# Kernel tuning notes

Hardware: AMD Instinct MI355X
Metric: run time of the kernel (lower is better)

Reference implementation:

```python
import jax, jax.numpy as jnp
import numpy as np

QBITS = 8  # fake-quant bit width from q_config
DT_RANK = 128
D_STATE = 16


def fake_quant_tensor(x, bits=QBITS):
    """Per-tensor symmetric fake quantization (quantize-dequantize) with STE."""
    qmax = 2.0 ** (bits - 1) - 1.0
    s = jnp.maximum(jnp.max(jnp.abs(x)) / qmax, 1e-8)
    q = jnp.clip(jnp.round(x / s), -qmax - 1.0, qmax) * s
    return x + jax.lax.stop_gradient(q - x)


def fake_quant_per_channel(w, bits=QBITS):
    """Per-output-channel symmetric fake quantization for weights [out, in]."""
    qmax = 2.0 ** (bits - 1) - 1.0
    s = jnp.maximum(jnp.max(jnp.abs(w), axis=-1, keepdims=True) / qmax, 1e-8)
    q = jnp.clip(jnp.round(w / s), -qmax - 1.0, qmax) * s
    return w + jax.lax.stop_gradient(q - w)


def setup_inputs() -> dict:
    key = jax.random.key(0)
    ks = jax.random.split(key, 8)
    B, L, D_MODEL = 2, 4096, 2048
    d_inner = D_MODEL  # expand = 1.0
    x = jax.random.normal(ks[0], (B, L, D_MODEL), jnp.float32)
    prompt = 0.1 * jax.random.normal(ks[1], (B, L, D_STATE), jnp.float32)
    # x_proj: Linear(d_inner -> dt_rank + 2*d_state), no bias
    Wx = jax.random.normal(ks[2], (DT_RANK + 2 * D_STATE, d_inner), jnp.float32) / np.sqrt(d_inner)
    # dt_proj: Linear(dt_rank -> d_inner), with bias
    Wdt = jax.random.normal(ks[3], (d_inner, DT_RANK), jnp.float32) / np.sqrt(DT_RANK)
    bdt = 0.1 * jax.random.normal(ks[4], (d_inner,), jnp.float32)
    # S4D-real init for A_log, D skip param (standard Mamba selective-scan params)
    A_log = jnp.log(jnp.tile(jnp.arange(1, D_STATE + 1, dtype=jnp.float32), (d_inner, 1)))
    Dskip = jax.random.normal(ks[5], (d_inner,), jnp.float32)
    return dict(x=x, prompt=prompt, Wx=Wx, Wdt=Wdt, bdt=bdt, A_log=A_log, Dskip=Dskip)


def reference(x, prompt, Wx, Wdt, bdt, A_log, Dskip):
    # x_proj with fake-quantized weight, then split into dt / B / C
    x_dbl = jnp.einsum('bld,od->blo', x, fake_quant_per_channel(Wx))
    dts = x_dbl[..., :DT_RANK]
    Bs = x_dbl[..., DT_RANK:DT_RANK + D_STATE]
    Cs = x_dbl[..., DT_RANK + D_STATE:]
    # dt_proj with fake-quantized weight
    dts = jnp.einsum('blr,or->blo', dts, fake_quant_per_channel(Wdt)) + bdt
    # activation fake-quant of scan inputs
    u_q = fake_quant_tensor(x)          # [B, L, d_inner]
    dt_q = fake_quant_tensor(dts)       # [B, L, d_inner]
    B_q = fake_quant_tensor(Bs)         # [B, L, d_state]
    C_q = fake_quant_tensor(Cs + prompt)  # [B, L, d_state]
    # selective scan (quantized SSM weights A, D)
    A = -jnp.exp(fake_quant_per_channel(A_log))  # [d_inner, d_state]
    D_q = fake_quant_tensor(Dskip)               # [d_inner]
    dt = jax.nn.softplus(dt_q)

    def step(h, inp):
        u_t, dt_t, B_t, C_t = inp  # [B,d], [B,d], [B,n], [B,n]
        dA = jnp.exp(dt_t[:, :, None] * A)             # [B, d, n]
        dBu = (dt_t * u_t)[:, :, None] * B_t[:, None, :]
        h = dA * h + dBu                               # [B, d, n]
        y = jnp.einsum('bdn,bn->bd', h, C_t)
        return h, y

    Bsz, L, d = x.shape
    h0 = jnp.zeros((Bsz, d, D_STATE), x.dtype)
    xs = (jnp.swapaxes(u_q, 0, 1), jnp.swapaxes(dt, 0, 1),
          jnp.swapaxes(B_q, 0, 1), jnp.swapaxes(C_q, 0, 1))
    _, ys = jax.lax.scan(step, h0, xs)  # ys: [L, B, d]
    return jnp.swapaxes(ys, 0, 1) + u_q * D_q
```

## Files before the change

kernel.cpp:

```cpp
#include <hip/hip_runtime.h>
#include <hip/hip_bf16.h>

#define BSZ    2
#define LSEQ   4096
#define DMODEL 2048
#define DTR    128
#define DST    16
#define ODIM   160
#define MROWS  (BSZ*LSEQ)
#define CH     64
#define TT     (LSEQ/CH)
#define LOG2E  1.44269504088896340736f
#define LN2    0.69314718055994530942f

typedef short  short8  __attribute__((ext_vector_type(8)));
typedef float  floatx4 __attribute__((ext_vector_type(4)));

__device__ __forceinline__ unsigned short f2bf(float f) {
    unsigned u = __float_as_uint(f);
    u += 0x7fffu + ((u >> 16) & 1u);
    return (unsigned short)(u >> 16);
}
__device__ __forceinline__ float quantv(float x, float s, float inv_s) {
    float q = rintf(x * inv_s);
    q = fminf(fmaxf(q, -128.0f), 127.0f);
    return q * s;
}
__device__ __forceinline__ float softplus_fast(float v) {
    float t = __builtin_amdgcn_exp2f(-fabsf(v) * LOG2E);
    return fmaxf(v, 0.0f) + LN2 * __log2f(1.0f + t);
}
__device__ __forceinline__ float scale_from_bits(unsigned bits) {
    return fmaxf(__uint_as_float(bits) * (1.0f/127.0f), 1e-8f);
}
__device__ __forceinline__ int pidx(int r, int k, int K) {
    return (r >> 4)*(16*K) + ((k >> 5) << 9) + (((r & 15) + (((k & 31) >> 3) << 4)) << 3) + (k & 7);
}

#define PB_WX  160
#define PB_WDT 128
#define PB_A   128
#define PB_D   1
#define PREP_BLOCKS (PB_WX + PB_WDT + PB_A + PB_D)

__global__ __launch_bounds__(256) void k_prep(
    const float* __restrict__ Wx, const float* __restrict__ Wdt,
    const float* __restrict__ A_log, const float* __restrict__ Dskip,
    unsigned short* __restrict__ Wxq, unsigned short* __restrict__ Wdtq,
    float* __restrict__ a2, float* __restrict__ Dq)
{
    int bid = blockIdx.x, tid = threadIdx.x;
    __shared__ float red[256];
    if (bid < PB_WX) {
        int o = bid, base = o * DMODEL;
        float m = 0.0f;
        for (int i = tid; i < DMODEL; i += 256) m = fmaxf(m, fabsf(Wx[base+i]));
        red[tid] = m; __syncthreads();
        for (int s2 = 128; s2 > 0; s2 >>= 1) { if (tid < s2) red[tid] = fmaxf(red[tid], red[tid+s2]); __syncthreads(); }
        float s = fmaxf(red[0]*(1.0f/127.0f), 1e-8f), inv = 1.0f/s;
        for (int i = tid; i < DMODEL; i += 256)
            Wxq[pidx(o, i, DMODEL)] = f2bf(quantv(Wx[base+i], s, inv));
    } else if (bid < PB_WX + PB_WDT) {
        int n = (bid - PB_WX)*16 + (tid >> 4);
        int k0 = (tid & 15)*8;
        const float* src = Wdt + (size_t)n*DTR + k0;
        float4 v0 = *reinterpret_cast<const float4*>(src);
        float4 v1 = *reinterpret_cast<const float4*>(src + 4);
        float m = fmaxf(fmaxf(fmaxf(fabsf(v0.x), fabsf(v0.y)), fmaxf(fabsf(v0.z), fabsf(v0.w))),
                        fmaxf(fmaxf(fabsf(v1.x), fabsf(v1.y)), fmaxf(fabsf(v1.z), fabsf(v1.w))));
        for (int off = 1; off < 16; off <<= 1) m = fmaxf(m, __shfl_xor(m, off, 16));
        float s = fmaxf(m*(1.0f/127.0f), 1e-8f), inv = 1.0f/s;
        short8 o8;
        o8[0]=(short)f2bf(quantv(v0.x,s,inv)); o8[1]=(short)f2bf(quantv(v0.y,s,inv));
        o8[2]=(short)f2bf(quantv(v0.z,s,inv)); o8[3]=(short)f2bf(quantv(v0.w,s,inv));
        o8[4]=(short)f2bf(quantv(v1.x,s,inv)); o8[5]=(short)f2bf(quantv(v1.y,s,inv));
        o8[6]=(short)f2bf(quantv(v1.z,s,inv)); o8[7]=(short)f2bf(quantv(v1.w,s,inv));
        *reinterpret_cast<short8*>(Wdtq + pidx(n, k0, DTR)) = o8;
    } else if (bid < PB_WX + PB_WDT + PB_A) {
        int d = (bid - PB_WX - PB_WDT)*16 + (tid >> 4);
        int n = tid & 15;
        float v = A_log[d*DST + n];
        float m = fabsf(v);
        for (int off = 1; off < 16; off <<= 1) m = fmaxf(m, __shfl_xor(m, off, 16));
        float s = fmaxf(m*(1.0f/127.0f), 1e-8f);
        float q = quantv(v, s, 1.0f/s);
        a2[d*DST + n] = -expf(q) * LOG2E;
    } else {
        float m = 0.0f;
        for (int i = tid; i < DMODEL; i += 256) m = fmaxf(m, fabsf(Dskip[i]));
        red[tid] = m; __syncthreads();
        for (int s2 = 128; s2 > 0; s2 >>= 1) { if (tid < s2) red[tid] = fmaxf(red[tid], red[tid+s2]); __syncthreads(); }
        float s = fmaxf(red[0]*(1.0f/127.0f), 1e-8f), inv = 1.0f/s;
        for (int i = tid; i < DMODEL; i += 256) Dq[i] = quantv(Dskip[i], s, inv);
    }
}

__global__ __launch_bounds__(256) void k_mm1(
    const float* __restrict__ x, const unsigned short* __restrict__ Wxq,
    const float* __restrict__ prompt,
    unsigned short* __restrict__ xdblbf, float* __restrict__ xbc,
    unsigned* __restrict__ scales)
{
    int tid = threadIdx.x, w = tid >> 6, lane = tid & 63;
    int mrow = lane & 15, quad = lane >> 4;
    int mt = blockIdx.x, m0 = mt*16, k0 = w*512;
    floatx4 acc[10] = {};
    float xmax = 0.0f;
    const float* arow = x + (size_t)(m0 + mrow)*DMODEL + k0 + quad*8;
    for (int kk = 0; kk < 512; kk += 32) {
        const float4* ap = reinterpret_cast<const float4*>(arow + kk);
        float4 a0 = ap[0], a1 = ap[1];
        xmax = fmaxf(xmax, fmaxf(fmaxf(fabsf(a0.x), fabsf(a0.y)), fmaxf(fabsf(a0.z), fabsf(a0.w))));
        xmax = fmaxf(xmax, fmaxf(fmaxf(fabsf(a1.x), fabsf(a1.y)), fmaxf(fabsf(a1.z), fabsf(a1.w))));
        short8 af;
        af[0]=(short)f2bf(a0.x); af[1]=(short)f2bf(a0.y); af[2]=(short)f2bf(a0.z); af[3]=(short)f2bf(a0.w);
        af[4]=(short)f2bf(a1.x); af[5]=(short)f2bf(a1.y); af[6]=(short)f2bf(a1.z); af[7]=(short)f2bf(a1.w);
        int kcidx = (k0 + kk) >> 5;
        #pragma unroll
        for (int j = 0; j < 10; ++j) {
            short8 bf = *reinterpret_cast<const short8*>(Wxq + j*16*DMODEL + kcidx*512 + lane*8);
            acc[j] = __builtin_amdgcn_mfma_f32_16x16x32_bf16(af, bf, acc[j], 0, 0, 0);
        }
    }
    for (int off = 32; off; off >>= 1) xmax = fmaxf(xmax, __shfl_xor(xmax, off, 64));
    __shared__ float red[4*2560];
    __shared__ float redB[256], redC[256];
    __shared__ float wred[4];
    if (lane == 0) wred[w] = xmax;
    #pragma unroll
    for (int j = 0; j < 10; ++j) {
        float4 v = make_float4(acc[j][0], acc[j][1], acc[j][2], acc[j][3]);
        *reinterpret_cast<float4*>(&red[w*2560 + (j*16 + mrow)*16 + quad*4]) = v;
    }
    __syncthreads();
    float bmax = 0.0f, cmax = 0.0f;
    #pragma unroll
    for (int j = 0; j < 10; ++j) {
        int e = j*256 + tid;
        float v = red[e] + red[2560+e] + red[5120+e] + red[7680+e];
        int col = e >> 4, rowin = e & 15, row = m0 + rowin;
        if (col < DTR) {
            xdblbf[mt*16*DTR + ((col>>5)<<9) + ((rowin + (((col&31)>>3)<<4))<<3) + (col&7)] = f2bf(v);
        } else if (col < DTR + DST) {
            bmax = fmaxf(bmax, fabsf(v));
            xbc[(size_t)row*32 + (col - DTR)] = v;
        } else {
            v += prompt[(size_t)row*DST + (col - DTR - DST)];
            cmax = fmaxf(cmax, fabsf(v));
            xbc[(size_t)row*32 + 16 + (col - DTR - DST)] = v;
        }
    }
    redB[tid] = bmax; redC[tid] = cmax; __syncthreads();
    for (int s2 = 128; s2 > 0; s2 >>= 1) {
        if (tid < s2) { redB[tid] = fmaxf(redB[tid], redB[tid+s2]); redC[tid] = fmaxf(redC[tid], redC[tid+s2]); }
        __syncthreads();
    }
    if (tid == 0) {
        atomicMax(&scales[0], __float_as_uint(fmaxf(fmaxf(wred[0], wred[1]), fmaxf(wred[2], wred[3]))));
        atomicMax(&scales[1], __float_as_uint(redB[0]));
        atomicMax(&scales[2], __float_as_uint(redC[0]));
    }
}

__global__ __launch_bounds__(256) void k_mm2(
    const unsigned short* __restrict__ Ap, const unsigned short* __restrict__ Bp,
    const float* __restrict__ bdt, float* __restrict__ dts, unsigned* __restrict__ scales)
{
    int tid = threadIdx.x, w = tid >> 6, lane = tid & 63;
    int mrow = lane & 15, quad = lane >> 4;
    int mt = blockIdx.x >> 4, nt = blockIdx.x & 15;
    int mtile = mt*4 + w, m0 = mtile*16, n0 = nt*128;
    short8 afr[4];
    const unsigned short* ab = Ap + (size_t)mtile*16*DTR + lane*8;
    #pragma unroll
    for (int kc = 0; kc < 4; ++kc) afr[kc] = *reinterpret_cast<const short8*>(ab + (kc<<9));
    floatx4 acc[8] = {};
    #pragma unroll
    for (int j = 0; j < 8; ++j) {
        const unsigned short* bb = Bp + (size_t)(n0/16 + j)*16*DTR + lane*8;
        #pragma unroll
        for (int kc = 0; kc < 4; ++kc) {
            short8 bf = *reinterpret_cast<const short8*>(bb + (kc<<9));
            acc[j] = __builtin_amdgcn_mfma_f32_16x16x32_bf16(afr[kc], bf, acc[j], 0, 0, 0);
        }
    }
    float dmax = 0.0f;
    #pragma unroll
    for (int j = 0; j < 8; ++j) {
        int col = n0 + j*16 + mrow;
        float bv = bdt[col];
        #pragma unroll
        for (int r = 0; r < 4; ++r) {
            int row = m0 + quad*4 + r;
            float v = acc[j][r] + bv;
            dmax = fmaxf(dmax, fabsf(v));
            dts[(size_t)row*DMODEL + col] = v;
        }
    }
    for (int off = 32; off; off >>= 1) dmax = fmaxf(dmax, __shfl_xor(dmax, off, 64));
    __shared__ float wd[4];
    if (lane == 0) wd[w] = dmax;
    __syncthreads();
    if (tid == 0)
        atomicMax(&scales[3], __float_as_uint(fmaxf(fmaxf(wd[0], wd[1]), fmaxf(wd[2], wd[3]))));
}

__global__ __launch_bounds__(256) void k_scan1(
    const float* __restrict__ dts, const float* __restrict__ x,
    const float* __restrict__ xbc, const float* __restrict__ a2,
    const unsigned* __restrict__ scales,
    float* __restrict__ Aprod, float* __restrict__ hfin)
{
    int bid = blockIdx.x, tid = threadIdx.x;
    int b = bid >> 9, rem = bid & 511, dblk = rem >> 6, ch = rem & 63;
    int d = dblk*256 + tid, t0 = ch*TT;
    float s_u  = scale_from_bits(scales[0]), inv_su  = 1.0f/s_u;
    float s_B  = scale_from_bits(scales[1]), inv_sB  = 1.0f/s_B;
    float s_dt = scale_from_bits(scales[3]), inv_sdt = 1.0f/s_dt;
    float a2r[16];
    {
        const float4* ap = reinterpret_cast<const float4*>(a2 + (size_t)d*DST);
        float4 v0 = ap[0], v1 = ap[1], v2 = ap[2], v3 = ap[3];
        a2r[0]=v0.x; a2r[1]=v0.y; a2r[2]=v0.z; a2r[3]=v0.w;
        a2r[4]=v1.x; a2r[5]=v1.y; a2r[6]=v1.z; a2r[7]=v1.w;
        a2r[8]=v2.x; a2r[9]=v2.y; a2r[10]=v2.z; a2r[11]=v2.w;
        a2r[12]=v3.x; a2r[13]=v3.y; a2r[14]=v3.z; a2r[15]=v3.w;
    }
    float h[16];
    #pragma unroll
    for (int n = 0; n < 16; ++n) h[n] = 0.0f;
    float sdt = 0.0f;
    __shared__ __align__(16) float Bq_p[8*16];
    for (int sub = 0; sub < TT/8; ++sub) {
        int tbase = t0 + sub*8;
        if (tid < 128) {
            int tb = tid >> 4, n = tid & 15;
            Bq_p[tid] = quantv(xbc[(size_t)(b*LSEQ + tbase + tb)*32 + n], s_B, inv_sB);
        }
        float dtr[8], ur[8];
        const float* pD = dts + (size_t)(b*LSEQ + tbase)*DMODEL + d;
        const float* pX = x   + (size_t)(b*LSEQ + tbase)*DMODEL + d;
        #pragma unroll
        for (int r = 0; r < 8; ++r) { dtr[r] = pD[(size_t)r*DMODEL]; ur[r] = pX[(size_t)r*DMODEL]; }
        __syncthreads();
        #pragma unroll
        for (int r = 0; r < 8; ++r) {
            float dtq = quantv(dtr[r], s_dt, inv_sdt);
            float dtv = softplus_fast(dtq);
            float uq  = quantv(ur[r], s_u, inv_su);
            float dtu = dtv * uq;
            sdt += dtv;
            const float4* bq4 = reinterpret_cast<const float4*>(&Bq_p[r*16]);
            float4 b0 = bq4[0], b1 = bq4[1], b2 = bq4[2], b3 = bq4[3];
            float bq[16] = { b0.x,b0.y,b0.z,b0.w, b1.x,b1.y,b1.z,b1.w,
                             b2.x,b2.y,b2.z,b2.w, b3.x,b3.y,b3.z,b3.w };
            #pragma unroll
            for (int n = 0; n < 16; ++n) {
                float dA = __builtin_amdgcn_exp2f(a2r[n]*dtv);
                h[n] = fmaf(dA, h[n], dtu*bq[n]);
            }
        }
        __syncthreads();
    }
    size_t ob = ((size_t)((b*CH + ch)*DMODEL + d))*DST;
    #pragma unroll
    for (int i = 0; i < 4; ++i) {
        float4 av = make_float4(__builtin_amdgcn_exp2f(a2r[4*i+0]*sdt),
                                __builtin_amdgcn_exp2f(a2r[4*i+1]*sdt),
                                __builtin_amdgcn_exp2f(a2r[4*i+2]*sdt),
                                __builtin_amdgcn_exp2f(a2r[4*i+3]*sdt));
        float4 hv = make_float4(h[4*i+0], h[4*i+1], h[4*i+2], h[4*i+3]);
        *reinterpret_cast<float4*>(Aprod + ob + 4*i) = av;
        *reinterpret_cast<float4*>(hfin  + ob + 4*i) = hv;
    }
}

__global__ __launch_bounds__(256) void k_mid(
    float* __restrict__ Aprod, const float* __restrict__ hfin)
{
    int f = blockIdx.x*256 + threadIdx.x;
    int b = f >> 15, dn = f & 32767;
    size_t base = (size_t)b*CH*32768 + dn;
    float h = 0.0f;
    #pragma unroll 4
    for (int ch = 0; ch < CH; ++ch) {
        size_t o = base + (size_t)ch*32768;
        float a = Aprod[o], hf = hfin[o];
        Aprod[o] = h;
        h = fmaf(a, h, hf);
    }
}

__global__ __launch_bounds__(256) void k_scan3(
    float* __restrict__ io ,
    const float* __restrict__ x, const float* __restrict__ xbc,
    const float* __restrict__ a2, const float* __restrict__ Dq,
    const unsigned* __restrict__ scales, const float* __restrict__ hinit)
{
    int bid = blockIdx.x, tid = threadIdx.x;
    int b = bid >> 9, rem = bid & 511, dblk = rem >> 6, ch = rem & 63;
    int d = dblk*256 + tid, t0 = ch*TT;
    float s_u  = scale_from_bits(scales[0]), inv_su  = 1.0f/s_u;
    float s_B  = scale_from_bits(scales[1]), inv_sB  = 1.0f/s_B;
    float s_C  = scale_from_bits(scales[2]), inv_sC  = 1.0f/s_C;
    float s_dt = scale_from_bits(scales[3]), inv_sdt = 1.0f/s_dt;
    float dqd = Dq[d];
    float a2r[16];
    {
        const float4* ap = reinterpret_cast<const float4*>(a2 + (size_t)d*DST);
        float4 v0 = ap[0], v1 = ap[1], v2 = ap[2], v3 = ap[3];
        a2r[0]=v0.x; a2r[1]=v0.y; a2r[2]=v0.z; a2r[3]=v0.w;
        a2r[4]=v1.x; a2r[5]=v1.y; a2r[6]=v1.z; a2r[7]=v1.w;
        a2r[8]=v2.x; a2r[9]=v2.y; a2r[10]=v2.z; a2r[11]=v2.w;
        a2r[12]=v3.x; a2r[13]=v3.y; a2r[14]=v3.z; a2r[15]=v3.w;
    }
    size_t ob = ((size_t)((b*CH + ch)*DMODEL + d))*DST;
    float h[16];
    #pragma unroll
    for (int i = 0; i < 4; ++i) {
        float4 hv = *reinterpret_cast<const float4*>(hinit + ob + 4*i);
        h[4*i+0]=hv.x; h[4*i+1]=hv.y; h[4*i+2]=hv.z; h[4*i+3]=hv.w;
    }
    __shared__ __align__(16) float Bq_p[8*16];
    __shared__ __align__(16) float Cq_p[8*16];
    for (int sub = 0; sub < TT/8; ++sub) {
        int tbase = t0 + sub*8;
        if (tid < 128) {
            int tb = tid >> 4, n = tid & 15;
            size_t pidx2 = (size_t)(b*LSEQ + tbase + tb)*32;
            Bq_p[tid] = quantv(xbc[pidx2 + n],      s_B, inv_sB);
            Cq_p[tid] = quantv(xbc[pidx2 + 16 + n], s_C, inv_sC);
        }
        float dtr[8], ur[8];
        float* pD = io + (size_t)(b*LSEQ + tbase)*DMODEL + d;
        const float* pX = x + (size_t)(b*LSEQ + tbase)*DMODEL + d;
        #pragma unroll
        for (int r = 0; r < 8; ++r) { dtr[r] = pD[(size_t)r*DMODEL]; ur[r] = pX[(size_t)r*DMODEL]; }
        __syncthreads();
        #pragma unroll
        for (int r = 0; r < 8; ++r) {
            float dtq = quantv(dtr[r], s_dt, inv_sdt);
            float dtv = softplus_fast(dtq);
            float uq  = quantv(ur[r], s_u, inv_su);
            float dtu = dtv * uq;
            const float4* bq4 = reinterpret_cast<const float4*>(&Bq_p[r*16]);
            const float4* cq4 = reinterpret_cast<const float4*>(&Cq_p[r*16]);
            float4 b0 = bq4[0], b1 = bq4[1], b2 = bq4[2], b3 = bq4[3];
            float4 c0 = cq4[0], c1 = cq4[1], c2 = cq4[2], c3 = cq4[3];
            float bq[16] = { b0.x,b0.y,b0.z,b0.w, b1.x,b1.y,b1.z,b1.w,
                             b2.x,b2.y,b2.z,b2.w, b3.x,b3.y,b3.z,b3.w };
            float cq[16] = { c0.x,c0.y,c0.z,c0.w, c1.x,c1.y,c1.z,c1.w,
                             c2.x,c2.y,c2.z,c2.w, c3.x,c3.y,c3.z,c3.w };
            float y = 0.0f;
            #pragma unroll
            for (int n = 0; n < 16; ++n) {
                float dA = __builtin_amdgcn_exp2f(a2r[n]*dtv);
                h[n] = fmaf(dA, h[n], dtu*bq[n]);
                y = fmaf(h[n], cq[n], y);
            }
            pD[(size_t)r*DMODEL] = y + uq * dqd;
        }
        __syncthreads();
    }
}

extern "C" void kernel_launch(void* const* d_in, const int* in_sizes, int n_in,
                              void* d_out, int out_size, void* d_ws, size_t ws_size,
                              hipStream_t stream)
{
    const float* x      = (const float*)d_in[0];
    const float* prompt = (const float*)d_in[1];
    const float* Wx     = (const float*)d_in[2];
    const float* Wdt    = (const float*)d_in[3];
    const float* bdt    = (const float*)d_in[4];
    const float* A_log  = (const float*)d_in[5];
    const float* Dskip  = (const float*)d_in[6];
    float* out = (float*)d_out;
    char* ws = (char*)d_ws;
    size_t off = 0;
    unsigned* scales       = (unsigned*)(ws + off);        off += 256;
    unsigned short* Wxq    = (unsigned short*)(ws + off);  off += (size_t)ODIM*DMODEL*2;
    unsigned short* Wdtq   = (unsigned short*)(ws + off);  off += (size_t)DMODEL*DTR*2;
    float* a2              = (float*)(ws + off);           off += (size_t)DMODEL*DST*4;
    float* Dq              = (float*)(ws + off);           off += (size_t)DMODEL*4;
    float* xbc             = (float*)(ws + off);           off += (size_t)MROWS*32*4;
    unsigned short* xdblbf = (unsigned short*)(ws + off);  off += (size_t)MROWS*DTR*2;
    float* Aprod           = (float*)(ws + off);           off += (size_t)BSZ*CH*DMODEL*DST*4;
    float* hfin            = (float*)(ws + off);           off += (size_t)BSZ*CH*DMODEL*DST*4;

    hipMemsetAsync(scales, 0, 256, stream);
    hipLaunchKernelGGL(k_prep, dim3(PREP_BLOCKS), dim3(256), 0, stream,
                       Wx, Wdt, A_log, Dskip, Wxq, Wdtq, a2, Dq);
    hipLaunchKernelGGL(k_mm1, dim3(MROWS/16), dim3(256), 0, stream,
                       x, Wxq, prompt, xdblbf, xbc, scales);
    hipLaunchKernelGGL(k_mm2, dim3((MROWS/64)*(DMODEL/128)), dim3(256), 0, stream,
                       xdblbf, Wdtq, bdt, out, scales);
    hipLaunchKernelGGL(k_scan1, dim3(BSZ*8*CH), dim3(256), 0, stream,
                       out, x, xbc, a2, scales, Aprod, hfin);
    hipLaunchKernelGGL(k_mid, dim3(BSZ*DMODEL*DST/256), dim3(256), 0, stream,
                       Aprod, hfin);
    hipLaunchKernelGGL(k_scan3, dim3(BSZ*8*CH), dim3(256), 0, stream,
                       out, x, xbc, a2, Dq, scales, Aprod);
}
```

Baseline: 300.2 us.

## Recompute dt projection inside scan kernels and pre-quantize u to int8

The dt_proj GEMM no longer writes the full fp32 dts tensor; k_mm2 becomes k_dmaxu, which only computes the dt abs-max and also writes x quantized to int8. Both scan passes recompute their dts tile with MFMA from the bf16 x_dbl and Wdt into LDS, and read the int8 u instead of fp32 x. This removes a 64MB fp32 write plus two 64MB reads, and shrinks u traffic fourfold. In exchange the GEMM runs three times, LDS use per block grows to about 42KB, and the output uses nontemporal stores.

```diff
diff --git a/kernel.cpp b/kernel.cpp
--- a/kernel.cpp
+++ b/kernel.cpp
@@ -162,40 +162,45 @@
     }
 }
 
-__global__ __launch_bounds__(256) void k_mm2(
+__global__ __launch_bounds__(256) void k_dmaxu(
     const unsigned short* __restrict__ Ap, const unsigned short* __restrict__ Bp,
-    const float* __restrict__ bdt, float* __restrict__ dts, unsigned* __restrict__ scales)
+    const float* __restrict__ bdt, const float* __restrict__ x,
+    signed char* __restrict__ u8, unsigned* __restrict__ scales)
 {
     int tid = threadIdx.x, w = tid >> 6, lane = tid & 63;
-    int mrow = lane & 15, quad = lane >> 4;
+    int mrow = lane & 15;
     int mt = blockIdx.x >> 4, nt = blockIdx.x & 15;
-    int mtile = mt*4 + w, m0 = mtile*16, n0 = nt*128;
+    int mtile = mt*4 + w, n0 = nt*128;
     short8 afr[4];
     const unsigned short* ab = Ap + (size_t)mtile*16*DTR + lane*8;
     #pragma unroll
     for (int kc = 0; kc < 4; ++kc) afr[kc] = *reinterpret_cast<const short8*>(ab + (kc<<9));
-    floatx4 acc[8] = {};
+    float dmax = 0.0f;
     #pragma unroll
     for (int j = 0; j < 8; ++j) {
         const unsigned short* bb = Bp + (size_t)(n0/16 + j)*16*DTR + lane*8;
+        floatx4 acc = {};
         #pragma unroll
         for (int kc = 0; kc < 4; ++kc) {
             short8 bf = *reinterpret_cast<const short8*>(bb + (kc<<9));
-            acc[j] = __builtin_amdgcn_mfma_f32_16x16x32_bf16(afr[kc], bf, acc[j], 0, 0, 0);
-        }
-    }
-    float dmax = 0.0f;
-    #pragma unroll
-    for (int j = 0; j < 8; ++j) {
-        int col = n0 + j*16 + mrow;
-        float bv = bdt[col];
-        #pragma unroll
-        for (int r = 0; r < 4; ++r) {
-            int row = m0 + quad*4 + r;
-            float v = acc[j][r] + bv;
-            dmax = fmaxf(dmax, fabsf(v));
-            dts[(size_t)row*DMODEL + col] = v;
-        }
+            acc = __builtin_amdgcn_mfma_f32_16x16x32_bf16(afr[kc], bf, acc, 0, 0, 0);
+        }
+        float bv = bdt[n0 + j*16 + mrow];
+        #pragma unroll
+        for (int r = 0; r < 4; ++r) dmax = fmaxf(dmax, fabsf(acc[r] + bv));
+    }
+    float s_u = scale_from_bits(scales[0]);
+    float inv_su = 1.0f / s_u;
+    const float4* xs = reinterpret_cast<const float4*>(x) + (size_t)blockIdx.x*2048;
+    unsigned* uo = reinterpret_cast<unsigned*>(u8) + (size_t)blockIdx.x*2048;
+    #pragma unroll
+    for (int i = 0; i < 8; ++i) {
+        float4 v = xs[i*256 + tid];
+        int q0 = (int)fminf(fmaxf(rintf(v.x*inv_su), -128.0f), 127.0f);
+        int q1 = (int)fminf(fmaxf(rintf(v.y*inv_su), -128.0f), 127.0f);
+        int q2 = (int)fminf(fmaxf(rintf(v.z*inv_su), -128.0f), 127.0f);
+        int q3 = (int)fminf(fmaxf(rintf(v.w*inv_su), -128.0f), 127.0f);
+        uo[i*256 + tid] = (q0 & 255) | ((q1 & 255) << 8) | ((q2 & 255) << 16) | ((unsigned)(q3 & 255) << 24);
     }
     for (int off = 32; off; off >>= 1) dmax = fmaxf(dmax, __shfl_xor(dmax, off, 64));
     __shared__ float wd[4];
@@ -206,15 +211,19 @@
 }
 
 __global__ __launch_bounds__(256) void k_scan1(
-    const float* __restrict__ dts, const float* __restrict__ x,
+    const unsigned short* __restrict__ Ap, const unsigned short* __restrict__ Bp,
+    const float* __restrict__ bdt, const signed char* __restrict__ u8,
     const float* __restrict__ xbc, const float* __restrict__ a2,
     const unsigned* __restrict__ scales,
     float* __restrict__ Aprod, float* __restrict__ hfin)
 {
     int bid = blockIdx.x, tid = threadIdx.x;
+    int w = tid >> 6, lane = tid & 63;
+    int mrow = lane & 15, quad = lane >> 4;
     int b = bid >> 9, rem = bid & 511, dblk = rem >> 6, ch = rem & 63;
-    int d = dblk*256 + tid, t0 = ch*TT;
-    float s_u  = scale_from_bits(scales[0]), inv_su  = 1.0f/s_u;
+    int d0 = dblk*256, t0 = ch*TT;
+    int d = d0 + tid;
+    float s_u  = scale_from_bits(scales[0]);
     float s_B  = scale_from_bits(scales[1]), inv_sB  = 1.0f/s_B;
     float s_dt = scale_from_bits(scales[3]), inv_sdt = 1.0f/s_dt;
     float a2r[16];
@@ -230,27 +239,59 @@
     #pragma unroll
     for (int n = 0; n < 16; ++n) h[n] = 0.0f;
     float sdt = 0.0f;
-    __shared__ __align__(16) float Bq_p[8*16];
-    for (int sub = 0; sub < TT/8; ++sub) {
-        int tbase = t0 + sub*8;
-        if (tid < 128) {
-            int tb = tid >> 4, n = tid & 15;
-            Bq_p[tid] = quantv(xbc[(size_t)(b*LSEQ + tbase + tb)*32 + n], s_B, inv_sB);
-        }
-        float dtr[8], ur[8];
-        const float* pD = dts + (size_t)(b*LSEQ + tbase)*DMODEL + d;
-        const float* pX = x   + (size_t)(b*LSEQ + tbase)*DMODEL + d;
-        #pragma unroll
-        for (int r = 0; r < 8; ++r) { dtr[r] = pD[(size_t)r*DMODEL]; ur[r] = pX[(size_t)r*DMODEL]; }
+    __shared__ float lds_dts[32*256];
+    __shared__ unsigned lds_u[32*64];
+    __shared__ __align__(16) float Bq_p[32*16];
+    for (int st = 0; st < 2; ++st) {
+        int tb = t0 + st*32;
+        int gm0 = (b*LSEQ + tb) >> 4;
+        short8 afr[2][4];
+        #pragma unroll
+        for (int rt = 0; rt < 2; ++rt)
+            #pragma unroll
+            for (int kc = 0; kc < 4; ++kc)
+                afr[rt][kc] = *reinterpret_cast<const short8*>(Ap + (size_t)(gm0+rt)*16*DTR + (kc<<9) + lane*8);
+        #pragma unroll
+        for (int j = 0; j < 4; ++j) {
+            int ntile = dblk*16 + w*4 + j;
+            int dloc = w*64 + j*16 + mrow;
+            float bdtv = bdt[d0 + dloc];
+            short8 bfr[4];
+            #pragma unroll
+            for (int kc = 0; kc < 4; ++kc)
+                bfr[kc] = *reinterpret_cast<const short8*>(Bp + (size_t)ntile*16*DTR + (kc<<9) + lane*8);
+            #pragma unroll
+            for (int rt = 0; rt < 2; ++rt) {
+                floatx4 acc = {};
+                #pragma unroll
+                for (int kc = 0; kc < 4; ++kc)
+                    acc = __builtin_amdgcn_mfma_f32_16x16x32_bf16(afr[rt][kc], bfr[kc], acc, 0, 0, 0);
+                #pragma unroll
+                for (int r = 0; r < 4; ++r)
+                    lds_dts[(rt*16 + quad*4 + r)*256 + dloc] = acc[r] + bdtv;
+            }
+        }
+        {
+            const unsigned* ub = reinterpret_cast<const unsigned*>(u8 + (size_t)(b*LSEQ + tb)*DMODEL + d0);
+            #pragma unroll
+            for (int i = 0; i < 8; ++i) {
+                int q = i*256 + tid;
+                lds_u[q] = ub[(q >> 6)*(DMODEL/4) + (q & 63)];
+            }
+            int e = tid;
+            Bq_p[e] = quantv(xbc[(size_t)(b*LSEQ + tb + (e>>4))*32 + (e&15)], s_B, inv_sB);
+            e = tid + 256;
+            Bq_p[e] = quantv(xbc[(size_t)(b*LSEQ + tb + (e>>4))*32 + (e&15)], s_B, inv_sB);
+        }
         __syncthreads();
-        #pragma unroll
-        for (int r = 0; r < 8; ++r) {
-            float dtq = quantv(dtr[r], s_dt, inv_sdt);
+        const signed char* lub = reinterpret_cast<const signed char*>(lds_u);
+        for (int t = 0; t < 32; ++t) {
+            float dtq = quantv(lds_dts[t*256 + tid], s_dt, inv_sdt);
             float dtv = softplus_fast(dtq);
-            float uq  = quantv(ur[r], s_u, inv_su);
+            float uq  = s_u * (float)lub[t*256 + tid];
             float dtu = dtv * uq;
             sdt += dtv;
-            const float4* bq4 = reinterpret_cast<const float4*>(&Bq_p[r*16]);
+            const float4* bq4 = reinterpret_cast<const float4*>(&Bq_p[t*16]);
             float4 b0 = bq4[0], b1 = bq4[1], b2 = bq4[2], b3 = bq4[3];
             float bq[16] = { b0.x,b0.y,b0.z,b0.w, b1.x,b1.y,b1.z,b1.w,
                              b2.x,b2.y,b2.z,b2.w, b3.x,b3.y,b3.z,b3.w };
@@ -292,15 +333,19 @@
 }
 
 __global__ __launch_bounds__(256) void k_scan3(
-    float* __restrict__ io ,
-    const float* __restrict__ x, const float* __restrict__ xbc,
-    const float* __restrict__ a2, const float* __restrict__ Dq,
-    const unsigned* __restrict__ scales, const float* __restrict__ hinit)
+    const unsigned short* __restrict__ Ap, const unsigned short* __restrict__ Bp,
+    const float* __restrict__ bdt, const signed char* __restrict__ u8,
+    const float* __restrict__ xbc, const float* __restrict__ a2,
+    const float* __restrict__ Dq, const unsigned* __restrict__ scales,
+    const float* __restrict__ hinit, float* __restrict__ out)
 {
     int bid = blockIdx.x, tid = threadIdx.x;
+    int w = tid >> 6, lane = tid & 63;
+    int mrow = lane & 15, quad = lane >> 4;
     int b = bid >> 9, rem = bid & 511, dblk = rem >> 6, ch = rem & 63;
-    int d = dblk*256 + tid, t0 = ch*TT;
-    float s_u  = scale_from_bits(scales[0]), inv_su  = 1.0f/s_u;
+    int d0 = dblk*256, t0 = ch*TT;
+    int d = d0 + tid;
+    float s_u  = scale_from_bits(scales[0]);
     float s_B  = scale_from_bits(scales[1]), inv_sB  = 1.0f/s_B;
     float s_C  = scale_from_bits(scales[2]), inv_sC  = 1.0f/s_C;
     float s_dt = scale_from_bits(scales[3]), inv_sdt = 1.0f/s_dt;
@@ -321,30 +366,64 @@
         float4 hv = *reinterpret_cast<const float4*>(hinit + ob + 4*i);
         h[4*i+0]=hv.x; h[4*i+1]=hv.y; h[4*i+2]=hv.z; h[4*i+3]=hv.w;
     }
-    __shared__ __align__(16) float Bq_p[8*16];
-    __shared__ __align__(16) float Cq_p[8*16];
-    for (int sub = 0; sub < TT/8; ++sub) {
-        int tbase = t0 + sub*8;
-        if (tid < 128) {
-            int tb = tid >> 4, n = tid & 15;
-            size_t pidx2 = (size_t)(b*LSEQ + tbase + tb)*32;
-            Bq_p[tid] = quantv(xbc[pidx2 + n],      s_B, inv_sB);
-            Cq_p[tid] = quantv(xbc[pidx2 + 16 + n], s_C, inv_sC);
-        }
-        float dtr[8], ur[8];
-        float* pD = io + (size_t)(b*LSEQ + tbase)*DMODEL + d;
-        const float* pX = x + (size_t)(b*LSEQ + tbase)*DMODEL + d;
-        #pragma unroll
-        for (int r = 0; r < 8; ++r) { dtr[r] = pD[(size_t)r*DMODEL]; ur[r] = pX[(size_t)r*DMODEL]; }
+    __shared__ float lds_dts[32*256];
+    __shared__ unsigned lds_u[32*64];
+    __shared__ __align__(16) float Bq_p[32*16];
+    __shared__ __align__(16) float Cq_p[32*16];
+    for (int st = 0; st < 2; ++st) {
+        int tb = t0 + st*32;
+        int gm0 = (b*LSEQ + tb) >> 4;
+        short8 afr[2][4];
+        #pragma unroll
+        for (int rt = 0; rt < 2; ++rt)
+            #pragma unroll
+            for (int kc = 0; kc < 4; ++kc)
+                afr[rt][kc] = *reinterpret_cast<const short8*>(Ap + (size_t)(gm0+rt)*16*DTR + (kc<<9) + lane*8);
+        #pragma unroll
+        for (int j = 0; j < 4; ++j) {
+            int ntile = dblk*16 + w*4 + j;
+            int dloc = w*64 + j*16 + mrow;
+            float bdtv = bdt[d0 + dloc];
+            short8 bfr[4];
+            #pragma unroll
+            for (int kc = 0; kc < 4; ++kc)
+                bfr[kc] = *reinterpret_cast<const short8*>(Bp + (size_t)ntile*16*DTR + (kc<<9) + lane*8);
+            #pragma unroll
+            for (int rt = 0; rt < 2; ++rt) {
+                floatx4 acc = {};
+                #pragma unroll
+                for (int kc = 0; kc < 4; ++kc)
+                    acc = __builtin_amdgcn_mfma_f32_16x16x32_bf16(afr[rt][kc], bfr[kc], acc, 0, 0, 0);
+                #pragma unroll
+                for (int r = 0; r < 4; ++r)
+                    lds_dts[(rt*16 + quad*4 + r)*256 + dloc] = acc[r] + bdtv;
+            }
+        }
+        {
+            const unsigned* ub = reinterpret_cast<const unsigned*>(u8 + (size_t)(b*LSEQ + tb)*DMODEL + d0);
+            #pragma unroll
+            for (int i = 0; i < 8; ++i) {
+                int q = i*256 + tid;
+                lds_u[q] = ub[(q >> 6)*(DMODEL/4) + (q & 63)];
+            }
+            int e = tid;
+            size_t px = (size_t)(b*LSEQ + tb + (e>>4))*32;
+            Bq_p[e] = quantv(xbc[px + (e&15)],      s_B, inv_sB);
+            Cq_p[e] = quantv(xbc[px + 16 + (e&15)], s_C, inv_sC);
+            e = tid + 256;
+            px = (size_t)(b*LSEQ + tb + (e>>4))*32;
+            Bq_p[e] = quantv(xbc[px + (e&15)],      s_B, inv_sB);
+            Cq_p[e] = quantv(xbc[px + 16 + (e&15)], s_C, inv_sC);
+        }
         __syncthreads();
-        #pragma unroll
-        for (int r = 0; r < 8; ++r) {
-            float dtq = quantv(dtr[r], s_dt, inv_sdt);
+        const signed char* lub = reinterpret_cast<const signed char*>(lds_u);
+        for (int t = 0; t < 32; ++t) {
+            float dtq = quantv(lds_dts[t*256 + tid], s_dt, inv_sdt);
             float dtv = softplus_fast(dtq);
-            float uq  = quantv(ur[r], s_u, inv_su);
+            float uq  = s_u * (float)lub[t*256 + tid];
             float dtu = dtv * uq;
-            const float4* bq4 = reinterpret_cast<const float4*>(&Bq_p[r*16]);
-            const float4* cq4 = reinterpret_cast<const float4*>(&Cq_p[r*16]);
+            const float4* bq4 = reinterpret_cast<const float4*>(&Bq_p[t*16]);
+            const float4* cq4 = reinterpret_cast<const float4*>(&Cq_p[t*16]);
             float4 b0 = bq4[0], b1 = bq4[1], b2 = bq4[2], b3 = bq4[3];
             float4 c0 = cq4[0], c1 = cq4[1], c2 = cq4[2], c3 = cq4[3];
             float bq[16] = { b0.x,b0.y,b0.z,b0.w, b1.x,b1.y,b1.z,b1.w,
@@ -358,7 +437,7 @@
                 h[n] = fmaf(dA, h[n], dtu*bq[n]);
                 y = fmaf(h[n], cq[n], y);
             }
-            pD[(size_t)r*DMODEL] = y + uq * dqd;
+            __builtin_nontemporal_store(y + uq * dqd, out + (size_t)(b*LSEQ + tb + t)*DMODEL + d);
         }
         __syncthreads();
     }
@@ -385,6 +464,7 @@
     float* Dq              = (float*)(ws + off);           off += (size_t)DMODEL*4;
     float* xbc             = (float*)(ws + off);           off += (size_t)MROWS*32*4;
     unsigned short* xdblbf = (unsigned short*)(ws + off);  off += (size_t)MROWS*DTR*2;
+    signed char* u8        = (signed char*)(ws + off);     off += (size_t)MROWS*DMODEL;
     float* Aprod           = (float*)(ws + off);           off += (size_t)BSZ*CH*DMODEL*DST*4;
     float* hfin            = (float*)(ws + off);           off += (size_t)BSZ*CH*DMODEL*DST*4;
 
@@ -393,12 +473,12 @@
                        Wx, Wdt, A_log, Dskip, Wxq, Wdtq, a2, Dq);
     hipLaunchKernelGGL(k_mm1, dim3(MROWS/16), dim3(256), 0, stream,
                        x, Wxq, prompt, xdblbf, xbc, scales);
-    hipLaunchKernelGGL(k_mm2, dim3((MROWS/64)*(DMODEL/128)), dim3(256), 0, stream,
-                       xdblbf, Wdtq, bdt, out, scales);
+    hipLaunchKernelGGL(k_dmaxu, dim3((MROWS/64)*(DMODEL/128)), dim3(256), 0, stream,
+                       xdblbf, Wdtq, bdt, x, u8, scales);
     hipLaunchKernelGGL(k_scan1, dim3(BSZ*8*CH), dim3(256), 0, stream,
-                       out, x, xbc, a2, scales, Aprod, hfin);
+                       xdblbf, Wdtq, bdt, u8, xbc, a2, scales, Aprod, hfin);
     hipLaunchKernelGGL(k_mid, dim3(BSZ*DMODEL*DST/256), dim3(256), 0, stream,
                        Aprod, hfin);
     hipLaunchKernelGGL(k_scan3, dim3(BSZ*8*CH), dim3(256), 0, stream,
-                       out, x, xbc, a2, Dq, scales, Aprod);
-}
+                       xdblbf, Wdtq, bdt, u8, xbc, a2, Dq, scales, Aprod, out);
+}
```

Result: slower. 309.7 us (+3.2%).
